# Optimization experiments

Measured on AMD Instinct MI355X. Metric: run time of the kernel, lower is better.

Reference implementation:

```python
import jax, jax.numpy as jnp
import numpy as np


def _gcn_norm(edge_index, num_nodes):
    # PyG GCNConv: add self-loops, symmetric normalization D^-1/2 (A+I) D^-1/2
    src, dst = edge_index[0], edge_index[1]
    loop = jnp.arange(num_nodes, dtype=edge_index.dtype)
    src = jnp.concatenate([src, loop])
    dst = jnp.concatenate([dst, loop])
    deg = jnp.zeros((num_nodes,), jnp.float32).at[dst].add(1.0)
    dinv = jnp.where(deg > 0, jax.lax.rsqrt(deg), 0.0)
    norm = dinv[src] * dinv[dst]  # [E + N]
    return src, dst, norm


def _gcn_conv(x, src, dst, norm, W, b):
    h = x @ W                                    # [N, out] dense GEMM first
    msg = h[src] * norm[:, None]                  # gather + scale, [E+N, out]
    agg = jax.ops.segment_sum(msg, dst, num_segments=x.shape[0])
    return agg + b


def setup_inputs() -> dict:
    key = jax.random.key(0)
    ks = jax.random.split(key, 8)
    N, E, F, H1, H2, C = 100000, 1600000, 128, 128, 128, 40
    s = 1.0 / np.sqrt(F)
    return {
        "x": jax.random.normal(ks[0], (N, F), jnp.float32),
        "edge_index": jax.random.randint(ks[1], (2, E), 0, N, jnp.int64),
        "W1": jax.random.normal(ks[2], (F, H1), jnp.float32) * s,
        "b1": jnp.zeros((H1,), jnp.float32),
        "W2": jax.random.normal(ks[3], (H1, H2), jnp.float32) * s,
        "b2": jnp.zeros((H2,), jnp.float32),
        "W3": jax.random.normal(ks[4], (H2, C), jnp.float32) * s,
        "b3": jnp.zeros((C,), jnp.float32),
    }


def reference(x, edge_index, W1, b1, W2, b2, W3, b3):
    N = x.shape[0]
    src, dst, norm = _gcn_norm(edge_index, N)
    h = jax.nn.relu(_gcn_conv(x, src, dst, norm, W1, b1))  # dropout is identity in eval
    h = jax.nn.relu(_gcn_conv(h, src, dst, norm, W2, b2))
    h = _gcn_conv(h, src, dst, norm, W3, b3)
    return jax.nn.log_softmax(h, axis=1)
```

## Files before the change

### kernel.cpp

```cpp
#include <hip/hip_runtime.h>
#include <hip/hip_bf16.h>
#include <math.h>

typedef short bf16x8 __attribute__((ext_vector_type(8)));
typedef unsigned short us8 __attribute__((ext_vector_type(8)));
typedef float f32x4 __attribute__((ext_vector_type(4)));

__device__ __forceinline__ float bf2f(unsigned short u) {
    return __uint_as_float(((unsigned)u) << 16);
}
__device__ __forceinline__ unsigned short f2bf(float f) {
    unsigned u = __float_as_uint(f);
    return (unsigned short)((u + 0x7FFF + ((u >> 16) & 1)) >> 16);
}

__global__ void ell_scatter(const int* __restrict__ ei, int* __restrict__ cnt,
                            int* __restrict__ ell, int E) {
    int base = blockIdx.x * 1024 + threadIdx.x;
    int s[4], d[4], idx[4];
#pragma unroll
    for (int j = 0; j < 4; j++) {
        int e = base + j * 256;
        bool v = e < E;
        s[j] = v ? ei[e] : -1;
        d[j] = v ? ei[E + e] : 0;
    }
#pragma unroll
    for (int j = 0; j < 4; j++)
        if (s[j] >= 0) idx[j] = atomicAdd(&cnt[d[j]], 1);
#pragma unroll
    for (int j = 0; j < 4; j++)
        if (s[j] >= 0 && idx[j] < 64) ell[(d[j] << 6) + idx[j]] = s[j];
}

__global__ void dinv_kernel(const int* __restrict__ cnt, float* __restrict__ dinv, int N) {
    int v = blockIdx.x * blockDim.x + threadIdx.x;
    if (v < N) dinv[v] = rsqrtf((float)(cnt[v] + 1));
}

struct TW {
    const float* src[3];
    unsigned short* dst[3];
    int C[3];
};
__global__ __launch_bounds__(256) void transposeW(TW tw) {
    __shared__ float Ts[128 * 128];
    int b = blockIdx.x;
    const float* W = tw.src[b];
    unsigned short* WT = tw.dst[b];
    int C = tw.C[b];
    int t = threadIdx.x;
    for (int i = t; i < 128 * C; i += 256) Ts[i] = W[i];
    __syncthreads();
    for (int i = t; i < C * 128; i += 256) {
        int c = i >> 7, k = i & 127;
        WT[c * 128 + k] = f2bf(Ts[k * C + c]);
    }
}

template<int NT, int NCOL, bool FP32IN>
__global__ __launch_bounds__(256) void gemm_mfma(const void* __restrict__ Xin,
                                                 const unsigned short* __restrict__ WT,
                                                 const float* __restrict__ dinv,
                                                 unsigned short* __restrict__ Hout, int N) {
    __shared__ unsigned short Ws[NT * 16 * 128];
    __shared__ unsigned short Xs[64 * 128];
    int t = threadIdx.x;
    int row0 = blockIdx.x * 64;
    for (int i = t; i < NT * 16 * 16; i += 256) {
        int r = i >> 4, s = i & 15;
        us8 val = (us8)0;
        if (r < NCOL) val = *(const us8*)&WT[r * 128 + s * 8];
        int byte = (r * 256) + ((s * 16) ^ ((r & 7) << 4));
        *(us8*)((char*)Ws + byte) = val;
    }
    for (int i = t; i < 64 * 16; i += 256) {
        int r = i >> 4, s = i & 15;
        int gr = row0 + r;
        us8 val = (us8)0;
        if (gr < N) {
            if (FP32IN) {
                const float4* Xf = (const float4*)Xin;
                float4 f0 = Xf[(size_t)gr * 32 + s * 2];
                float4 f1 = Xf[(size_t)gr * 32 + s * 2 + 1];
                val[0] = f2bf(f0.x); val[1] = f2bf(f0.y); val[2] = f2bf(f0.z); val[3] = f2bf(f0.w);
                val[4] = f2bf(f1.x); val[5] = f2bf(f1.y); val[6] = f2bf(f1.z); val[7] = f2bf(f1.w);
            } else {
                const unsigned short* Xh = (const unsigned short*)Xin;
                val = *(const us8*)&Xh[(size_t)gr * 128 + s * 8];
            }
        }
        int byte = (r * 256) + ((s * 16) ^ ((r & 7) << 4));
        *(us8*)((char*)Xs + byte) = val;
    }
    __syncthreads();

    int wid = t >> 6, lane = t & 63;
    int arow = wid * 16 + (lane & 15);
    f32x4 acc[NT];
#pragma unroll
    for (int i = 0; i < NT; i++) acc[i] = 0.0f;

#pragma unroll
    for (int kk = 0; kk < 4; kk++) {
        int kbyte = kk * 64 + (lane >> 4) * 16;
        bf16x8 a = *(const bf16x8*)((const char*)Xs + (arow * 256) + (kbyte ^ ((arow & 7) << 4)));
#pragma unroll
        for (int ct = 0; ct < NT; ct++) {
            int brow = ct * 16 + (lane & 15);
            bf16x8 b = *(const bf16x8*)((const char*)Ws + (brow * 256) + (kbyte ^ ((brow & 7) << 4)));
            acc[ct] = __builtin_amdgcn_mfma_f32_16x16x32_bf16(a, b, acc[ct], 0, 0, 0);
        }
    }
    int dcol = lane & 15;
    int drow = wid * 16 + (lane >> 4) * 4;
#pragma unroll
    for (int ct = 0; ct < NT; ct++) {
        int col = ct * 16 + dcol;
#pragma unroll
        for (int j = 0; j < 4; j++) {
            int grow = row0 + drow + j;
            if (grow < N && col < NCOL)
                Hout[(size_t)grow * NCOL + col] = f2bf(acc[ct][j] * dinv[grow]);
        }
    }
}

__global__ __launch_bounds__(256) void agg128_b(const ushort4* __restrict__ Hp,
                                                const int* __restrict__ cnt,
                                                const int* __restrict__ ell,
                                                const float* __restrict__ dinv,
                                                const float* __restrict__ bias,
                                                ushort4* __restrict__ Hout, int N) {
    int r = blockIdx.x * 8 + (threadIdx.x >> 5);
    if (r >= N) return;
    int lane = threadIdx.x & 31;
    int deg = min(cnt[r], 64);
    const int* nb = &ell[r << 6];
    ushort4 sv = Hp[(size_t)r * 32 + lane];
    float a0 = bf2f(sv.x), a1 = bf2f(sv.y), a2 = bf2f(sv.z), a3 = bf2f(sv.w);
    int p = 0;
    for (; p + 8 <= deg; p += 8) {
        int s0 = nb[p + 0], s1 = nb[p + 1], s2 = nb[p + 2], s3 = nb[p + 3];
        int s4 = nb[p + 4], s5 = nb[p + 5], s6 = nb[p + 6], s7 = nb[p + 7];
        ushort4 v0 = Hp[(size_t)s0 * 32 + lane];
        ushort4 v1 = Hp[(size_t)s1 * 32 + lane];
        ushort4 v2 = Hp[(size_t)s2 * 32 + lane];
        ushort4 v3 = Hp[(size_t)s3 * 32 + lane];
        ushort4 v4 = Hp[(size_t)s4 * 32 + lane];
        ushort4 v5 = Hp[(size_t)s5 * 32 + lane];
        ushort4 v6 = Hp[(size_t)s6 * 32 + lane];
        ushort4 v7 = Hp[(size_t)s7 * 32 + lane];
        a0 += bf2f(v0.x) + bf2f(v1.x) + bf2f(v2.x) + bf2f(v3.x)
            + bf2f(v4.x) + bf2f(v5.x) + bf2f(v6.x) + bf2f(v7.x);
        a1 += bf2f(v0.y) + bf2f(v1.y) + bf2f(v2.y) + bf2f(v3.y)
            + bf2f(v4.y) + bf2f(v5.y) + bf2f(v6.y) + bf2f(v7.y);
        a2 += bf2f(v0.z) + bf2f(v1.z) + bf2f(v2.z) + bf2f(v3.z)
            + bf2f(v4.z) + bf2f(v5.z) + bf2f(v6.z) + bf2f(v7.z);
        a3 += bf2f(v0.w) + bf2f(v1.w) + bf2f(v2.w) + bf2f(v3.w)
            + bf2f(v4.w) + bf2f(v5.w) + bf2f(v6.w) + bf2f(v7.w);
    }
    for (; p < deg; ++p) {
        int s = nb[p];
        ushort4 v = Hp[(size_t)s * 32 + lane];
        a0 += bf2f(v.x); a1 += bf2f(v.y); a2 += bf2f(v.z); a3 += bf2f(v.w);
    }
    float dv = dinv[r];
    float o0 = fmaxf(a0 * dv + bias[lane * 4 + 0], 0.f);
    float o1 = fmaxf(a1 * dv + bias[lane * 4 + 1], 0.f);
    float o2 = fmaxf(a2 * dv + bias[lane * 4 + 2], 0.f);
    float o3 = fmaxf(a3 * dv + bias[lane * 4 + 3], 0.f);
    ushort4 o; o.x = f2bf(o0); o.y = f2bf(o1); o.z = f2bf(o2); o.w = f2bf(o3);
    Hout[(size_t)r * 32 + lane] = o;
}

__global__ __launch_bounds__(256) void agg40_lsm(const ushort4* __restrict__ Gs,
                                                 const int* __restrict__ cnt,
                                                 const int* __restrict__ ell,
                                                 const float* __restrict__ dinv,
                                                 const float* __restrict__ b3,
                                                 float* __restrict__ Out, int N) {
    int t = threadIdx.x;
    int wv = t >> 6;
    int lw = t & 63;
    int g = lw / 10;
    int l = lw - g * 10;
    if (g >= 6) return;
    int r = blockIdx.x * 24 + wv * 6 + g;
    if (r >= N) return;
    int deg = min(cnt[r], 64);
    const int* nb = &ell[r << 6];
    ushort4 sv = Gs[(size_t)r * 10 + l];
    float a0 = bf2f(sv.x), a1 = bf2f(sv.y), a2 = bf2f(sv.z), a3 = bf2f(sv.w);
    int p = 0;
    for (; p + 4 <= deg; p += 4) {
        int s0 = nb[p], s1 = nb[p + 1], s2 = nb[p + 2], s3 = nb[p + 3];
        ushort4 v0 = Gs[(size_t)s0 * 10 + l];
        ushort4 v1 = Gs[(size_t)s1 * 10 + l];
        ushort4 v2 = Gs[(size_t)s2 * 10 + l];
        ushort4 v3 = Gs[(size_t)s3 * 10 + l];
        a0 += bf2f(v0.x) + bf2f(v1.x) + bf2f(v2.x) + bf2f(v3.x);
        a1 += bf2f(v0.y) + bf2f(v1.y) + bf2f(v2.y) + bf2f(v3.y);
        a2 += bf2f(v0.z) + bf2f(v1.z) + bf2f(v2.z) + bf2f(v3.z);
        a3 += bf2f(v0.w) + bf2f(v1.w) + bf2f(v2.w) + bf2f(v3.w);
    }
    for (; p < deg; ++p) {
        int s = nb[p];
        ushort4 v = Gs[(size_t)s * 10 + l];
        a0 += bf2f(v.x); a1 += bf2f(v.y); a2 += bf2f(v.z); a3 += bf2f(v.w);
    }
    float dv = dinv[r];
    float v0 = a0 * dv + b3[4 * l + 0];
    float v1 = a1 * dv + b3[4 * l + 1];
    float v2 = a2 * dv + b3[4 * l + 2];
    float v3 = a3 * dv + b3[4 * l + 3];
    float m4 = fmaxf(fmaxf(v0, v1), fmaxf(v2, v3));
    float m = m4;
#pragma unroll
    for (int k = 1; k < 10; k++)
        m = fmaxf(m, __shfl(m4, g * 10 + ((l + k) % 10), 64));
    float e4 = expf(v0 - m) + expf(v1 - m) + expf(v2 - m) + expf(v3 - m);
    float ssum = e4;
#pragma unroll
    for (int k = 1; k < 10; k++)
        ssum += __shfl(e4, g * 10 + ((l + k) % 10), 64);
    float lse = m + logf(ssum);
    float4 o = make_float4(v0 - lse, v1 - lse, v2 - lse, v3 - lse);
    *(float4*)&Out[(size_t)r * 40 + 4 * l] = o;
}

extern "C" void kernel_launch(void* const* d_in, const int* in_sizes, int n_in,
                              void* d_out, int out_size, void* d_ws, size_t ws_size,
                              hipStream_t stream) {
    const float* x  = (const float*)d_in[0];
    const int*   ei = (const int*)d_in[1];
    const float* W1 = (const float*)d_in[2];
    const float* b1 = (const float*)d_in[3];
    const float* W2 = (const float*)d_in[4];
    const float* b2 = (const float*)d_in[5];
    const float* W3 = (const float*)d_in[6];
    const float* b3 = (const float*)d_in[7];
    float* out = (float*)d_out;

    const int N = in_sizes[0] / 128;
    const int E = in_sizes[1] / 2;

    auto align = [](size_t v) { return (v + 255) & ~(size_t)255; };
    char* w = (char*)d_ws;
    size_t off = 0;
    unsigned short* bufA = (unsigned short*)(w + off); off += align((size_t)N * 128 * 2);
    unsigned short* bufB = (unsigned short*)(w + off); off += align((size_t)N * 128 * 2);
    unsigned short* gs   = (unsigned short*)(w + off); off += align((size_t)N * 40 * 2);
    unsigned short* W1T  = (unsigned short*)(w + off); off += align(128 * 128 * 2);
    unsigned short* W2T  = (unsigned short*)(w + off); off += align(128 * 128 * 2);
    unsigned short* W3T  = (unsigned short*)(w + off); off += align(40 * 128 * 2);
    int* cnt  = (int*)(w + off);   off += align((size_t)N * 4);
    float* dinv = (float*)(w + off); off += align((size_t)N * 4);
    int* ellf = (int*)(w + off);   off += align((size_t)N * 64 * 4);

    hipMemsetAsync(cnt, 0, (size_t)N * 4, stream);

    TW tw;
    tw.src[0] = W1; tw.dst[0] = W1T; tw.C[0] = 128;
    tw.src[1] = W2; tw.dst[1] = W2T; tw.C[1] = 128;
    tw.src[2] = W3; tw.dst[2] = W3T; tw.C[2] = 40;
    transposeW<<<3, 256, 0, stream>>>(tw);

    ell_scatter<<<(E + 1023) / 1024, 256, 0, stream>>>(ei, cnt, ellf, E);
    dinv_kernel<<<(N + 255) / 256, 256, 0, stream>>>(cnt, dinv, N);

    int ggemm = (N + 63) / 64;
    int gagg  = (N + 7) / 8;
    gemm_mfma<8, 128, true><<<ggemm, 256, 0, stream>>>(x, W1T, dinv, bufA, N);
    agg128_b<<<gagg, 256, 0, stream>>>((const ushort4*)bufA, cnt, ellf, dinv, b1,
                                       (ushort4*)bufB, N);
    gemm_mfma<8, 128, false><<<ggemm, 256, 0, stream>>>(bufB, W2T, dinv, bufA, N);
    agg128_b<<<gagg, 256, 0, stream>>>((const ushort4*)bufA, cnt, ellf, dinv, b2,
                                       (ushort4*)bufB, N);
    gemm_mfma<3, 40, false><<<ggemm, 256, 0, stream>>>(bufB, W3T, dinv, gs, N);
    agg40_lsm<<<(N + 23) / 24, 256, 0, stream>>>((const ushort4*)gs, cnt, ellf, dinv,
                                                 b3, out, N);
}
```

Baseline: 471.9 us.

## Build ELL adjacency via bucketed counting-sort partition instead of global atomics

Replaces the single ELL scatter kernel, which did a global atomicAdd per edge into a per-node counter, with a multi-pass counting sort. Edges are histogrammed into 128-node buckets in shared memory, scanned, partitioned into a packed pairs array, and then expanded per bucket with shared-memory atomics that also write degree and dinv. This aims to cut contended random global atomics and scattered writes, but it adds four extra launches and reuses workspace buffers as scratch. It also assumes source ids fit in 17 bits, that there are at most 1024 buckets, and at most 256 edge chunks.

```diff
diff --git a/kernel.cpp b/kernel.cpp
--- a/kernel.cpp
+++ b/kernel.cpp
@@ -14,28 +14,111 @@
     return (unsigned short)((u + 0x7FFF + ((u >> 16) & 1)) >> 16);
 }
 
-__global__ void ell_scatter(const int* __restrict__ ei, int* __restrict__ cnt,
-                            int* __restrict__ ell, int E) {
-    int base = blockIdx.x * 1024 + threadIdx.x;
-    int s[4], d[4], idx[4];
+
+__global__ __launch_bounds__(256) void histA(const int* __restrict__ ei, int* __restrict__ ghist,
+                                             int NBUK, int E, int chunk) {
+    __shared__ int lh[1024];
+    int t = threadIdx.x;
+    for (int i = t; i < NBUK; i += 256) lh[i] = 0;
+    __syncthreads();
+    int e0 = blockIdx.x * chunk;
+    int e1 = min(e0 + chunk, E);
+    for (int e = e0 + t; e < e1; e += 256)
+        atomicAdd(&lh[ei[E + e] >> 7], 1);
+    __syncthreads();
+    for (int i = t; i < NBUK; i += 256) ghist[blockIdx.x * NBUK + i] = lh[i];
+}
+
+__global__ __launch_bounds__(256) void scanB1(int* __restrict__ ghist, int* __restrict__ buktot,
+                                              int NBUK, int NBLK) {
+    __shared__ int sd[256];
+    int buk = blockIdx.x, t = threadIdx.x;
+    int v = (t < NBLK) ? ghist[t * NBUK + buk] : 0;
+    sd[t] = v;
+    __syncthreads();
+    for (int off = 1; off < 256; off <<= 1) {
+        int x = (t >= off) ? sd[t - off] : 0;
+        __syncthreads();
+        sd[t] += x;
+        __syncthreads();
+    }
+    if (t < NBLK) ghist[t * NBUK + buk] = sd[t] - v;
+    if (t == 255) buktot[buk] = sd[255];
+}
+
+__global__ __launch_bounds__(256) void scanB2(const int* __restrict__ buktot,
+                                              int* __restrict__ bukbase, int NBUK) {
+    __shared__ int sd[256];
+    int t = threadIdx.x;
+    int v[4]; int s = 0;
 #pragma unroll
     for (int j = 0; j < 4; j++) {
-        int e = base + j * 256;
-        bool v = e < E;
-        s[j] = v ? ei[e] : -1;
-        d[j] = v ? ei[E + e] : 0;
-    }
-#pragma unroll
-    for (int j = 0; j < 4; j++)
-        if (s[j] >= 0) idx[j] = atomicAdd(&cnt[d[j]], 1);
-#pragma unroll
-    for (int j = 0; j < 4; j++)
-        if (s[j] >= 0 && idx[j] < 64) ell[(d[j] << 6) + idx[j]] = s[j];
-}
-
-__global__ void dinv_kernel(const int* __restrict__ cnt, float* __restrict__ dinv, int N) {
-    int v = blockIdx.x * blockDim.x + threadIdx.x;
-    if (v < N) dinv[v] = rsqrtf((float)(cnt[v] + 1));
+        int idx = t * 4 + j;
+        v[j] = (idx < NBUK) ? buktot[idx] : 0;
+        s += v[j];
+    }
+    sd[t] = s;
+    __syncthreads();
+    for (int off = 1; off < 256; off <<= 1) {
+        int x = (t >= off) ? sd[t - off] : 0;
+        __syncthreads();
+        sd[t] += x;
+        __syncthreads();
+    }
+    int run = sd[t] - s;
+#pragma unroll
+    for (int j = 0; j < 4; j++) {
+        int idx = t * 4 + j;
+        if (idx < NBUK) bukbase[idx] = run;
+        run += v[j];
+    }
+    if (t == 255) bukbase[NBUK] = sd[255];
+}
+
+__global__ __launch_bounds__(256) void partC(const int* __restrict__ ei,
+                                             const int* __restrict__ ghist,
+                                             const int* __restrict__ bukbase,
+                                             int* __restrict__ pairs,
+                                             int NBUK, int E, int chunk) {
+    __shared__ int lcur[1024];
+    int t = threadIdx.x, blk = blockIdx.x;
+    for (int i = t; i < NBUK; i += 256) lcur[i] = bukbase[i] + ghist[blk * NBUK + i];
+    __syncthreads();
+    int e0 = blk * chunk;
+    int e1 = min(e0 + chunk, E);
+    for (int e = e0 + t; e < e1; e += 256) {
+        int s = ei[e], d = ei[E + e];
+        int buk = d >> 7;
+        int pos = atomicAdd(&lcur[buk], 1);
+        pairs[pos] = s | ((d & 127) << 17);
+    }
+}
+
+__global__ __launch_bounds__(256) void expandD(const int* __restrict__ pairs,
+                                               const int* __restrict__ bukbase,
+                                               int* __restrict__ ell, int* __restrict__ cnt,
+                                               float* __restrict__ dinv, int N) {
+    __shared__ int lcnt[128];
+    int buk = blockIdx.x, t = threadIdx.x;
+    if (t < 128) lcnt[t] = 0;
+    __syncthreads();
+    int p0 = bukbase[buk], p1 = bukbase[buk + 1];
+    int nbase = buk << 7;
+    for (int p = p0 + t; p < p1; p += 256) {
+        int v = pairs[p];
+        int ld = v >> 17;
+        int idx = atomicAdd(&lcnt[ld], 1);
+        if (idx < 64) ell[((nbase + ld) << 6) + idx] = v & 0x1FFFF;
+    }
+    __syncthreads();
+    if (t < 128) {
+        int node = nbase + t;
+        if (node < N) {
+            int deg = lcnt[t];
+            cnt[node] = deg;
+            dinv[node] = rsqrtf((float)(deg + 1));
+        }
+    }
 }
 
 struct TW {
@@ -244,6 +327,9 @@
 
     const int N = in_sizes[0] / 128;
     const int E = in_sizes[1] / 2;
+    const int NBUK = (N + 127) >> 7;
+    int chunk = ((E + 249) / 250 + 255) & ~255;
+    const int NBLK = (E + chunk - 1) / chunk;
 
     auto align = [](size_t v) { return (v + 255) & ~(size_t)255; };
     char* w = (char*)d_ws;
@@ -258,7 +344,10 @@
     float* dinv = (float*)(w + off); off += align((size_t)N * 4);
     int* ellf = (int*)(w + off);   off += align((size_t)N * 64 * 4);
 
-    hipMemsetAsync(cnt, 0, (size_t)N * 4, stream);
+    int* pairs   = (int*)bufA;
+    int* ghist   = (int*)gs;
+    int* buktot  = ghist + (size_t)NBLK * NBUK;
+    int* bukbase = buktot + NBUK;
 
     TW tw;
     tw.src[0] = W1; tw.dst[0] = W1T; tw.C[0] = 128;
@@ -266,8 +355,11 @@
     tw.src[2] = W3; tw.dst[2] = W3T; tw.C[2] = 40;
     transposeW<<<3, 256, 0, stream>>>(tw);
 
-    ell_scatter<<<(E + 1023) / 1024, 256, 0, stream>>>(ei, cnt, ellf, E);
-    dinv_kernel<<<(N + 255) / 256, 256, 0, stream>>>(cnt, dinv, N);
+    histA<<<NBLK, 256, 0, stream>>>(ei, ghist, NBUK, E, chunk);
+    scanB1<<<NBUK, 256, 0, stream>>>(ghist, buktot, NBUK, NBLK);
+    scanB2<<<1, 256, 0, stream>>>(buktot, bukbase, NBUK);
+    partC<<<NBLK, 256, 0, stream>>>(ei, ghist, bukbase, pairs, NBUK, E, chunk);
+    expandD<<<NBUK, 256, 0, stream>>>(pairs, bukbase, ellf, cnt, dinv, N);
 
     int ggemm = (N + 63) / 64;
     int gagg  = (N + 7) / 8;
```

Measured after the change: 388.3 us. -17.7%, faster.
